# Performance work log

Measured on AMD Instinct MI355X. Metric: run time of the kernel, lower is better.

Reference implementation:

```python
import jax, jax.numpy as jnp
import numpy as np

T, B, E, H = 512, 32, 512, 2048

def setup_inputs() -> dict:
    key = jax.random.key(0)
    k1, k2, k3 = jax.random.split(key, 3)
    sent = jax.random.normal(k1, (T, B, E), dtype=jnp.float32)
    lengths = jax.random.randint(k2, (B,), 1, T + 1)  # unused by the math (pack is never applied)
    # Linear(E, 3H) params (PyTorch default-ish init scale)
    W = jax.random.normal(k3, (3 * H, E), dtype=jnp.float32) * (1.0 / np.sqrt(E))
    b = jnp.zeros((3 * H,), dtype=jnp.float32)
    return {"sent": sent, "lengths": lengths, "W": W, "b": b}

def reference(sent, lengths, W, b):
    # sent: (T, B, E) time-major. Single QRNN layer, window=1, output_gate=True, zoneout=0.
    Y = jnp.einsum('tbe,he->tbh', sent, W) + b          # (T, B, 3H)
    Z, F, O = jnp.split(Y, 3, axis=-1)
    Z = jnp.tanh(Z)
    F = jax.nn.sigmoid(F)
    O = jax.nn.sigmoid(O)

    # forget-mult recurrence: c_t = f_t * z_t + (1 - f_t) * c_{t-1}, c_0 = 0
    def step(c, zf):
        z, f = zf
        c = f * z + (1.0 - f) * c
        return c, c
    c0 = jnp.zeros_like(Z[0])                            # (B, H)
    _, C = jax.lax.scan(step, c0, (Z, F))                # (T, B, H)

    Hseq = O * C                                         # QRNN output (T, B, H)
    embeds = jnp.max(Hseq, axis=0)                       # torch.max(sent_output, 0)[0] -> (B, H)
    return embeds
```

## Files before the change

### kernel.cpp

```cpp
#include <hip/hip_runtime.h>
#include <stdint.h>

#define TT 512
#define BB 32
#define EE 512
#define HH 2048

typedef __attribute__((ext_vector_type(8))) short short8;
typedef __attribute__((ext_vector_type(4))) float f32x4;

#define XROW 528
#define XBUF (16 * XROW)

#define BAR_VM4() asm volatile("s_waitcnt vmcnt(4) lgkmcnt(0)\n\ts_barrier" ::: "memory")
#define BAR_VM0() asm volatile("s_waitcnt vmcnt(0) lgkmcnt(0)\n\ts_barrier" ::: "memory")

static __device__ __forceinline__ unsigned short f2bf(float f) {
    union { float f; unsigned u; } v; v.f = f;
    unsigned u = v.u;
    unsigned r = u + 0x7FFFu + ((u >> 16) & 1u);
    return (unsigned short)(r >> 16);
}

static __device__ __forceinline__ float fast_exp(float x) {
    return __builtin_amdgcn_exp2f(x * 1.44269504f);
}
static __device__ __forceinline__ float fast_rcp(float x) {
    return __builtin_amdgcn_rcpf(x);
}

static __device__ __forceinline__ void load_lds16(const unsigned short* g, unsigned short* l) {
    __builtin_amdgcn_global_load_lds(
        (const __attribute__((address_space(1))) unsigned int*)(uintptr_t)g,
        (__attribute__((address_space(3))) unsigned int*)(uintptr_t)l,
        16, 0, 0);
}

__global__ void convert_inputs(const float* __restrict__ X,
                               const float* __restrict__ W,
                               unsigned short* __restrict__ Xb,
                               unsigned short* __restrict__ Wb) {
    const int nX = TT * BB * EE;
    int i = (blockIdx.x * blockDim.x + threadIdx.x) * 8;
    const float* src;
    unsigned short* dst;
    int j;
    if (i < nX) { src = X; dst = Xb; j = i; }
    else        { src = W; dst = Wb; j = i - nX; }
    float4 v0 = *(const float4*)(src + j);
    float4 v1 = *(const float4*)(src + j + 4);
    union { short8 s; unsigned short u[8]; } o;
    o.u[0] = f2bf(v0.x); o.u[1] = f2bf(v0.y); o.u[2] = f2bf(v0.z); o.u[3] = f2bf(v0.w);
    o.u[4] = f2bf(v1.x); o.u[5] = f2bf(v1.y); o.u[6] = f2bf(v1.z); o.u[7] = f2bf(v1.w);
    *(short8*)(dst + j) = o.s;
}

__launch_bounds__(256, 2)
__global__ void qrnn_fused(const unsigned short* __restrict__ Xb,
                           const unsigned short* __restrict__ Wb,
                           const float* __restrict__ bias,
                           float* __restrict__ out)
{
    __shared__ unsigned short xlds[3 * XBUF];
    __shared__ float exch[2][2][64][12];

    const int tid  = threadIdx.x;
    const int wv   = tid >> 6;
    const int lane = tid & 63;
    const int q    = lane >> 4;
    const int c    = lane & 15;
    const int hi   = wv >> 1;
    const int s    = wv & 1;

    const int id   = blockIdx.x;
    const int xcd  = id & 7;
    const int slot = id >> 3;
    const int b    = xcd * 4 + (slot >> 6);
    const int hgrp = slot & 63;
    const int h    = hgrp * 32 + hi * 16 + c;

    short8 wz[8], wf[8], wo[8];
    {
        const unsigned short* wzr = Wb + (size_t)h * EE            + s * 256;
        const unsigned short* wfr = Wb + (size_t)(HH + h) * EE     + s * 256;
        const unsigned short* wor = Wb + (size_t)(2 * HH + h) * EE + s * 256;
#pragma unroll
        for (int k = 0; k < 8; ++k) {
            int e0 = k * 32 + q * 8;
            wz[k] = *(const short8*)(wzr + e0);
            wf[k] = *(const short8*)(wfr + e0);
            wo[k] = *(const short8*)(wor + e0);
        }
    }
#pragma unroll
    for (int k = 0; k < 8; ++k) {
        asm volatile("" : "+a"(wz[k]), "+a"(wf[k]), "+a"(wo[k]));
    }

    const float b0 = (s == 0) ? bias[h]          : 0.0f;
    const float b1 = (s == 0) ? bias[HH + h]     : 0.0f;
    const float b2 = (s == 0) ? bias[2 * HH + h] : 0.0f;

    float carry = 0.0f;
    float vmax  = -1e30f;

    const unsigned short* g0 = Xb + ((size_t)(wv * 4) * BB + b) * EE + lane * 8;
    unsigned short* l0 = &xlds[(wv * 4) * XROW];

    auto stage = [&](int n, int slt) {
        const unsigned short* g = g0 + (size_t)n * (16 * BB * EE);
        unsigned short* l = l0 + slt * XBUF;
#pragma unroll
        for (int i = 0; i < 4; ++i)
            load_lds16(g + (size_t)i * (BB * EE), l + i * XROW);
    };

    auto do_tail = [&](f32x4 az, f32x4 af, f32x4 ao) {
        float aa[4], mm[4], oo[4];
#pragma unroll
        for (int r = 0; r < 4; ++r) {
            float e2 = fast_exp(2.0f * az[r]);
            float z  = 1.0f - 2.0f * fast_rcp(e2 + 1.0f);
            float f  = fast_rcp(1.0f + fast_exp(-af[r]));
            float o  = fast_rcp(1.0f + fast_exp(-ao[r]));
            aa[r] = f * z;
            mm[r] = 1.0f - f;
            oo[r] = o;
        }

        float A = aa[0], M = mm[0];
#pragma unroll
        for (int r = 1; r < 4; ++r) { A = aa[r] + mm[r] * A; M = mm[r] * M; }

        float Ap = __shfl_up(A, 16, 64), Mp = __shfl_up(M, 16, 64);
        if (q >= 1) { A = A + M * Ap; M = M * Mp; }
        Ap = __shfl_up(A, 32, 64); Mp = __shfl_up(M, 32, 64);
        if (q >= 2) { A = A + M * Ap; M = M * Mp; }
        float Ae = __shfl_up(A, 16, 64), Me = __shfl_up(M, 16, 64);
        if (q == 0) { Ae = 0.0f; Me = 1.0f; }
        float cc = Ae + Me * carry;

#pragma unroll
        for (int r = 0; r < 4; ++r) {
            cc = aa[r] + mm[r] * cc;
            vmax = fmaxf(vmax, oo[r] * cc);
        }

        float cend = A + M * carry;
        carry = __shfl(cend, 48 + c, 64);
    };

    stage(0, 0);
    stage(1, 1);
    BAR_VM4();

    f32x4 prevz, prevf, prevo;

    for (int ch = 0; ch < 32; ++ch) {
        const int buf = ch % 3;
        if (ch < 30) stage(ch + 2, (ch + 2) % 3);

        const unsigned short* Abase = &xlds[buf * XBUF + c * XROW + s * 256 + q * 8];
        short8 a[8];
#pragma unroll
        for (int k = 0; k < 8; ++k)
            a[k] = *(const short8*)(Abase + k * 32);

        f32x4 pz, pf, po;
        if (s == 0 && ch > 0) {
            const float* e = &exch[(ch - 1) & 1][hi][lane][0];
            pz = *(const f32x4*)(e);
            pf = *(const f32x4*)(e + 4);
            po = *(const f32x4*)(e + 8);
        }

        f32x4 az = {b0, b0, b0, b0};
        f32x4 af = {b1, b1, b1, b1};
        f32x4 ao = {b2, b2, b2, b2};
#pragma unroll
        for (int k = 0; k < 8; ++k) {
            az = __builtin_amdgcn_mfma_f32_16x16x32_bf16(a[k], wz[k], az, 0, 0, 0);
            af = __builtin_amdgcn_mfma_f32_16x16x32_bf16(a[k], wf[k], af, 0, 0, 0);
            ao = __builtin_amdgcn_mfma_f32_16x16x32_bf16(a[k], wo[k], ao, 0, 0, 0);
        }

        if (s == 1) {
            float* e = &exch[ch & 1][hi][lane][0];
            *(f32x4*)(e)     = az;
            *(f32x4*)(e + 4) = af;
            *(f32x4*)(e + 8) = ao;
        }

        if (s == 0 && ch > 0) {
            do_tail(prevz + pz, prevf + pf, prevo + po);
        }

        prevz = az; prevf = af; prevo = ao;

        if (ch < 30) BAR_VM4(); else BAR_VM0();
    }

    if (s == 0) {
        const float* e = &exch[31 & 1][hi][lane][0];
        f32x4 pz = *(const f32x4*)(e);
        f32x4 pf = *(const f32x4*)(e + 4);
        f32x4 po = *(const f32x4*)(e + 8);
        do_tail(prevz + pz, prevf + pf, prevo + po);

        vmax = fmaxf(vmax, __shfl_xor(vmax, 16, 64));
        vmax = fmaxf(vmax, __shfl_xor(vmax, 32, 64));
        if (q == 0) out[(size_t)b * HH + h] = vmax;
    }
}

extern "C" void kernel_launch(void* const* d_in, const int* in_sizes, int n_in,
                              void* d_out, int out_size, void* d_ws, size_t ws_size,
                              hipStream_t stream) {
    const float* sent = (const float*)d_in[0];
    const float* W    = (const float*)d_in[2];
    const float* bias = (const float*)d_in[3];
    float* out        = (float*)d_out;

    const int nX = TT * BB * EE;
    const int nW = 3 * HH * EE;
    unsigned short* Xb = (unsigned short*)d_ws;
    unsigned short* Wb = Xb + nX;

    int totalVec = (nX + nW) / 8;
    convert_inputs<<<totalVec / 256, 256, 0, stream>>>(sent, W, Xb, Wb);

    dim3 grid(2048);
    qrnn_fused<<<grid, 256, 0, stream>>>(Xb, Wb, bias, out);
}
```

Measured before the change: 244.7 us.

## Symmetrize wave-pair partial exchange, split MFMA accumulators, use packed bf16 convert

Both K-half waves now write their partial Z/F/O sums to their own exchange slot and read the partner's, so each wave runs the scan tail redundantly. The s==1 waves no longer sit idle at the barrier while s==0 waves do the tail. Each gate's MFMA chain is split into two independent accumulators to shorten dependency chains, and the first chunk is peeled out of the loop. The input conversion switches to the hardware packed v_cvt_pk_bf16_f32 instruction. In exchange the shared exchange buffer doubles in size and the tail transcendentals are executed twice.

```diff
diff --git a/kernel.cpp b/kernel.cpp
--- a/kernel.cpp
+++ b/kernel.cpp
@@ -15,18 +15,17 @@
 #define BAR_VM4() asm volatile("s_waitcnt vmcnt(4) lgkmcnt(0)\n\ts_barrier" ::: "memory")
 #define BAR_VM0() asm volatile("s_waitcnt vmcnt(0) lgkmcnt(0)\n\ts_barrier" ::: "memory")
 
-static __device__ __forceinline__ unsigned short f2bf(float f) {
-    union { float f; unsigned u; } v; v.f = f;
-    unsigned u = v.u;
-    unsigned r = u + 0x7FFFu + ((u >> 16) & 1u);
-    return (unsigned short)(r >> 16);
-}
-
 static __device__ __forceinline__ float fast_exp(float x) {
     return __builtin_amdgcn_exp2f(x * 1.44269504f);
 }
 static __device__ __forceinline__ float fast_rcp(float x) {
     return __builtin_amdgcn_rcpf(x);
+}
+
+static __device__ __forceinline__ unsigned cvtpk_bf16(float lo, float hi) {
+    unsigned r;
+    asm("v_cvt_pk_bf16_f32 %0, %1, %2" : "=v"(r) : "v"(lo), "v"(hi));
+    return r;
 }
 
 static __device__ __forceinline__ void load_lds16(const unsigned short* g, unsigned short* l) {
@@ -49,9 +48,11 @@
     else        { src = W; dst = Wb; j = i - nX; }
     float4 v0 = *(const float4*)(src + j);
     float4 v1 = *(const float4*)(src + j + 4);
-    union { short8 s; unsigned short u[8]; } o;
-    o.u[0] = f2bf(v0.x); o.u[1] = f2bf(v0.y); o.u[2] = f2bf(v0.z); o.u[3] = f2bf(v0.w);
-    o.u[4] = f2bf(v1.x); o.u[5] = f2bf(v1.y); o.u[6] = f2bf(v1.z); o.u[7] = f2bf(v1.w);
+    union { short8 s; unsigned u[4]; } o;
+    o.u[0] = cvtpk_bf16(v0.x, v0.y);
+    o.u[1] = cvtpk_bf16(v0.z, v0.w);
+    o.u[2] = cvtpk_bf16(v1.x, v1.y);
+    o.u[3] = cvtpk_bf16(v1.z, v1.w);
     *(short8*)(dst + j) = o.s;
 }
 
@@ -62,7 +63,7 @@
                            float* __restrict__ out)
 {
     __shared__ unsigned short xlds[3 * XBUF];
-    __shared__ float exch[2][2][64][12];
+    __shared__ float exch[2][2][2][64][12];
 
     const int tid  = threadIdx.x;
     const int wv   = tid >> 6;
@@ -156,7 +157,37 @@
 
     f32x4 prevz, prevf, prevo;
 
-    for (int ch = 0; ch < 32; ++ch) {
+    {
+        stage(2, 2);
+        const unsigned short* Abase = &xlds[0 * XBUF + c * XROW + s * 256 + q * 8];
+        short8 a[8];
+#pragma unroll
+        for (int k = 0; k < 8; ++k)
+            a[k] = *(const short8*)(Abase + k * 32);
+
+        f32x4 az0 = {b0, b0, b0, b0}, az1 = {0.f, 0.f, 0.f, 0.f};
+        f32x4 af0 = {b1, b1, b1, b1}, af1 = {0.f, 0.f, 0.f, 0.f};
+        f32x4 ao0 = {b2, b2, b2, b2}, ao1 = {0.f, 0.f, 0.f, 0.f};
+#pragma unroll
+        for (int k = 0; k < 8; k += 2) {
+            az0 = __builtin_amdgcn_mfma_f32_16x16x32_bf16(a[k],     wz[k],     az0, 0, 0, 0);
+            az1 = __builtin_amdgcn_mfma_f32_16x16x32_bf16(a[k + 1], wz[k + 1], az1, 0, 0, 0);
+            af0 = __builtin_amdgcn_mfma_f32_16x16x32_bf16(a[k],     wf[k],     af0, 0, 0, 0);
+            af1 = __builtin_amdgcn_mfma_f32_16x16x32_bf16(a[k + 1], wf[k + 1], af1, 0, 0, 0);
+            ao0 = __builtin_amdgcn_mfma_f32_16x16x32_bf16(a[k],     wo[k],     ao0, 0, 0, 0);
+            ao1 = __builtin_amdgcn_mfma_f32_16x16x32_bf16(a[k + 1], wo[k + 1], ao1, 0, 0, 0);
+        }
+        prevz = az0 + az1; prevf = af0 + af1; prevo = ao0 + ao1;
+
+        float* w = &exch[0][hi][s][lane][0];
+        *(f32x4*)(w)     = prevz;
+        *(f32x4*)(w + 4) = prevf;
+        *(f32x4*)(w + 8) = prevo;
+
+        BAR_VM4();
+    }
+
+    for (int ch = 1; ch < 32; ++ch) {
         const int buf = ch % 3;
         if (ch < 30) stage(ch + 2, (ch + 2) % 3);
 
@@ -166,51 +197,48 @@
         for (int k = 0; k < 8; ++k)
             a[k] = *(const short8*)(Abase + k * 32);
 
-        f32x4 pz, pf, po;
-        if (s == 0 && ch > 0) {
-            const float* e = &exch[(ch - 1) & 1][hi][lane][0];
-            pz = *(const f32x4*)(e);
-            pf = *(const f32x4*)(e + 4);
-            po = *(const f32x4*)(e + 8);
-        }
-
-        f32x4 az = {b0, b0, b0, b0};
-        f32x4 af = {b1, b1, b1, b1};
-        f32x4 ao = {b2, b2, b2, b2};
-#pragma unroll
-        for (int k = 0; k < 8; ++k) {
-            az = __builtin_amdgcn_mfma_f32_16x16x32_bf16(a[k], wz[k], az, 0, 0, 0);
-            af = __builtin_amdgcn_mfma_f32_16x16x32_bf16(a[k], wf[k], af, 0, 0, 0);
-            ao = __builtin_amdgcn_mfma_f32_16x16x32_bf16(a[k], wo[k], ao, 0, 0, 0);
-        }
-
-        if (s == 1) {
-            float* e = &exch[ch & 1][hi][lane][0];
-            *(f32x4*)(e)     = az;
-            *(f32x4*)(e + 4) = af;
-            *(f32x4*)(e + 8) = ao;
-        }
-
-        if (s == 0 && ch > 0) {
-            do_tail(prevz + pz, prevf + pf, prevo + po);
-        }
+        const float* e = &exch[(ch - 1) & 1][hi][s ^ 1][lane][0];
+        f32x4 pz = *(const f32x4*)(e);
+        f32x4 pf = *(const f32x4*)(e + 4);
+        f32x4 po = *(const f32x4*)(e + 8);
+
+        f32x4 az0 = {b0, b0, b0, b0}, az1 = {0.f, 0.f, 0.f, 0.f};
+        f32x4 af0 = {b1, b1, b1, b1}, af1 = {0.f, 0.f, 0.f, 0.f};
+        f32x4 ao0 = {b2, b2, b2, b2}, ao1 = {0.f, 0.f, 0.f, 0.f};
+#pragma unroll
+        for (int k = 0; k < 8; k += 2) {
+            az0 = __builtin_amdgcn_mfma_f32_16x16x32_bf16(a[k],     wz[k],     az0, 0, 0, 0);
+            az1 = __builtin_amdgcn_mfma_f32_16x16x32_bf16(a[k + 1], wz[k + 1], az1, 0, 0, 0);
+            af0 = __builtin_amdgcn_mfma_f32_16x16x32_bf16(a[k],     wf[k],     af0, 0, 0, 0);
+            af1 = __builtin_amdgcn_mfma_f32_16x16x32_bf16(a[k + 1], wf[k + 1], af1, 0, 0, 0);
+            ao0 = __builtin_amdgcn_mfma_f32_16x16x32_bf16(a[k],     wo[k],     ao0, 0, 0, 0);
+            ao1 = __builtin_amdgcn_mfma_f32_16x16x32_bf16(a[k + 1], wo[k + 1], ao1, 0, 0, 0);
+        }
+        f32x4 az = az0 + az1, af = af0 + af1, ao = ao0 + ao1;
+
+        float* w = &exch[ch & 1][hi][s][lane][0];
+        *(f32x4*)(w)     = az;
+        *(f32x4*)(w + 4) = af;
+        *(f32x4*)(w + 8) = ao;
+
+        do_tail(prevz + pz, prevf + pf, prevo + po);
 
         prevz = az; prevf = af; prevo = ao;
 
         if (ch < 30) BAR_VM4(); else BAR_VM0();
     }
 
-    if (s == 0) {
-        const float* e = &exch[31 & 1][hi][lane][0];
+    {
+        const float* e = &exch[1][hi][s ^ 1][lane][0];
         f32x4 pz = *(const f32x4*)(e);
         f32x4 pf = *(const f32x4*)(e + 4);
         f32x4 po = *(const f32x4*)(e + 8);
         do_tail(prevz + pz, prevf + pf, prevo + po);
-
-        vmax = fmaxf(vmax, __shfl_xor(vmax, 16, 64));
-        vmax = fmaxf(vmax, __shfl_xor(vmax, 32, 64));
-        if (q == 0) out[(size_t)b * HH + h] = vmax;
-    }
+    }
+
+    vmax = fmaxf(vmax, __shfl_xor(vmax, 16, 64));
+    vmax = fmaxf(vmax, __shfl_xor(vmax, 32, 64));
+    if (s == 0 && q == 0) out[(size_t)b * HH + h] = vmax;
 }
 
 extern "C" void kernel_launch(void* const* d_in, const int* in_sizes, int n_in,
```

New measurement: 265.4 us. +8.5%, slower.
